# Kernel optimization log

Measured on AMD Instinct MI355X. Metric: run time of the kernel, lower is better.

The kernel has to match this reference:

```python
import jax, jax.numpy as jnp
import numpy as np

EMBED_DIM = 1024
HEAD_DIM = 64
B, T = 4, 4096


def setup_inputs() -> dict:
    key = jax.random.key(0)
    kx, kq, kk, kv = jax.random.split(key, 4)
    x = jax.random.normal(kx, (B, T, EMBED_DIM), dtype=jnp.float32)
    # nn.Linear weights, stored transposed as (in, out) for x @ W
    s = 1.0 / np.sqrt(EMBED_DIM)
    Wq = jax.random.normal(kq, (EMBED_DIM, HEAD_DIM), dtype=jnp.float32) * s
    Wk = jax.random.normal(kk, (EMBED_DIM, HEAD_DIM), dtype=jnp.float32) * s
    Wv = jax.random.normal(kv, (EMBED_DIM, HEAD_DIM), dtype=jnp.float32) * s
    return {"x": x, "Wq": Wq, "Wk": Wk, "Wv": Wv}


def reference(x, Wq, Wk, Wv):
    Bc, Tc, C = x.shape
    Q = x @ Wq  # [B, T, H]
    K = x @ Wk
    V = x @ Wv
    # NOTE: original scales by embedding_dim C, not head_dim
    scores = jnp.einsum('bqh,bkh->bqk', Q, K) / jnp.sqrt(jnp.float32(C))
    causal = jnp.tril(jnp.ones((Tc, Tc), dtype=bool))
    scores = jnp.where(causal, scores, -jnp.inf)
    attn = jax.nn.softmax(scores, axis=-1)
    return jnp.einsum('bqk,bkh->bqh', attn, V)
```

## Files before the change

kernel.cpp:

```cpp
#include <hip/hip_runtime.h>
#include <hip/hip_bf16.h>
#include <math.h>

typedef __attribute__((ext_vector_type(8))) short bf16x8;
typedef __attribute__((ext_vector_type(4))) float f32x4;

#define MFMA16 __builtin_amdgcn_mfma_f32_16x16x32_bf16

static constexpr int TSEQ = 4096;
static constexpr int EMB = 1024;
static constexpr int HD = 64;

__device__ __forceinline__ unsigned short f2bf(float f) {
    unsigned u = __builtin_bit_cast(unsigned, f);
    u += 0x7fffu + ((u >> 16) & 1u);
    return (unsigned short)(u >> 16);
}
__device__ __forceinline__ int pk2bf(float a, float b) {
    return (int)((unsigned)f2bf(a) | ((unsigned)f2bf(b) << 16));
}

union frag_u { int i[4]; bf16x8 v; };

__global__ void prep_w(const float* __restrict__ Wq, const float* __restrict__ Wk,
                       const float* __restrict__ Wv, unsigned short* __restrict__ Wp) {
    int id = blockIdx.x * 256 + threadIdx.x;
    int wsel = id >> 16;
    int t = id & 65535;
    int k = t >> 6, n0 = t & 63;
    const float* W = (wsel == 0) ? Wq : (wsel == 1) ? Wk : Wv;
    float v = W[t];
    if (wsel == 0) v *= 0.03125f;
    int n = wsel * 64 + n0;
    Wp[(k >> 5) * 6144 + n * 32 + (k & 31)] = f2bf(v);
}

__global__ __launch_bounds__(256, 2) void proj_kernel(const float* __restrict__ X,
        const unsigned short* __restrict__ Wp, unsigned short* __restrict__ Qp,
        unsigned short* __restrict__ Kp, unsigned short* __restrict__ Vp) {
    __shared__ unsigned short xt[2][32][64];
    const int tid = threadIdx.x;
    const int lane = tid & 63, wave = tid >> 6;
    const int col = lane & 15, quad = lane >> 4;
    const int rf = wave & 1, ch = wave >> 1;
    const int row0 = blockIdx.x * 32;

    const int srow = tid >> 3;
    const int spiece = tid & 7;
    const float* gx = X + (size_t)(row0 + srow) * EMB + spiece * 8;
    const int sdst = ((spiece ^ (srow & 7)) * 8);

    const int arow = rf * 16 + col;
    const int apu0 = (0 * 4 + quad) ^ (arow & 7);
    const int apu1 = (1 * 4 + quad) ^ (arow & 7);

    const int fragoff = col * 64 + quad * 16;
    const char* wB = (const char*)Wp + ch * 6 * 1024 + fragoff;

    f32x4 acc[6];
#pragma unroll
    for (int t = 0; t < 6; t++) acc[t] = (f32x4)(0.0f);

    {
        const float4 xa = *(const float4*)(gx);
        const float4 xb = *(const float4*)(gx + 4);
        frag_u u;
        u.i[0] = pk2bf(xa.x, xa.y); u.i[1] = pk2bf(xa.z, xa.w);
        u.i[2] = pk2bf(xb.x, xb.y); u.i[3] = pk2bf(xb.z, xb.w);
        *(bf16x8*)&xt[0][srow][sdst] = u.v;
    }
    __syncthreads();

    int buf = 0;
    for (int kc = 0; kc < 16; kc++) {
        float4 xa, xb;
        if (kc < 15) {
            const float* g = gx + (kc + 1) * 64;
            xa = *(const float4*)(g);
            xb = *(const float4*)(g + 4);
        }
        const bf16x8 a0 = *(const bf16x8*)&xt[buf][arow][apu0 * 8];
        const bf16x8 a1 = *(const bf16x8*)&xt[buf][arow][apu1 * 8];
        const char* wp = wB + kc * 24576;
#pragma unroll
        for (int cf = 0; cf < 6; cf++) {
            const bf16x8 w0 = *(const bf16x8*)(wp + cf * 1024);
            const bf16x8 w1 = *(const bf16x8*)(wp + 12288 + cf * 1024);
            acc[cf] = MFMA16(a0, w0, acc[cf], 0, 0, 0);
            acc[cf] = MFMA16(a1, w1, acc[cf], 0, 0, 0);
        }
        if (kc < 15) {
            frag_u u;
            u.i[0] = pk2bf(xa.x, xa.y); u.i[1] = pk2bf(xa.z, xa.w);
            u.i[2] = pk2bf(xb.x, xb.y); u.i[3] = pk2bf(xb.z, xb.w);
            *(bf16x8*)&xt[buf ^ 1][srow][sdst] = u.v;
        }
        __syncthreads();
        buf ^= 1;
    }

    const int tile = blockIdx.x * 2 + rf;
    const int c = blockIdx.x;
    const int j = rf;
#pragma unroll
    for (int cf = 0; cf < 6; cf++) {
        const int n0 = ch * 96 + cf * 16;
        if (n0 < 64) {
            const int t = n0 >> 4;
#pragma unroll
            for (int r = 0; r < 4; r++)
                Qp[tile * 1024 + (t >> 1) * 512 + (quad * 4 + r) * 32 +
                   ((t & 1) * 2 + (col >> 3)) * 8 + (col & 7)] = f2bf(acc[cf][r]);
        } else if (n0 < 128) {
            const int tt = (n0 - 64) >> 4;
#pragma unroll
            for (int r = 0; r < 4; r++)
                Kp[((c * 2 + j) * 2 + (tt >> 1)) * 512 + (quad * 4 + r) * 32 +
                   ((tt & 1) * 2 + (col >> 3)) * 8 + (col & 7)] = f2bf(acc[cf][r]);
        } else {
            const int t4 = (n0 - 128) >> 4;
            ushort4 pk;
            pk.x = f2bf(acc[cf][0]); pk.y = f2bf(acc[cf][1]);
            pk.z = f2bf(acc[cf][2]); pk.w = f2bf(acc[cf][3]);
            *(ushort4*)&Vp[c * 2048 + t4 * 512 + col * 32 + j * 16 + quad * 4] = pk;
        }
    }
}

__global__ __launch_bounds__(512, 4) void attn_kernel(const unsigned short* __restrict__ Qp,
        const unsigned short* __restrict__ Kp, const unsigned short* __restrict__ Vp,
        float* __restrict__ Out) {
    __shared__ float cmb[4][2][64][20];
    __shared__ unsigned short plds[8][2][640];
    const int lane = threadIdx.x & 63, wave = threadIdx.x >> 6;
    const int col = lane & 15, quad = lane >> 4;
    const int batch = blockIdx.x & 3;
    const int ti = 127 - (blockIdx.x >> 2);
    const int q0 = ti * 32;
    const size_t bT = (size_t)batch * TSEQ;
    const int fragoff = col * 64 + quad * 16;

    const char* QpB = (const char*)Qp;
    const char* KpB = (const char*)Kp;
    const char* VpB = (const char*)Vp;
    const int gt = (int)((bT + q0) >> 4);
    const int c0 = (int)(bT >> 5);

    bf16x8 aq[2][2];
#pragma unroll
    for (int m = 0; m < 2; m++)
#pragma unroll
        for (int h = 0; h < 2; h++)
            aq[m][h] = *(const bf16x8*)(QpB + (size_t)((gt + m) * 2 + h) * 1024 + fragoff);

    f32x4 o[2][4];
    f32x4 lsum[2];
#pragma unroll
    for (int m = 0; m < 2; m++) {
        lsum[m] = (f32x4)(0.0f);
#pragma unroll
        for (int t = 0; t < 4; t++) o[m][t] = (f32x4)(0.0f);
    }

    for (int c = wave; c <= ti; c += 8) {
        const char* kb = KpB + (size_t)(c0 + c) * 4096;
        const char* vb = VpB + (size_t)(c0 + c) * 4096;
        bf16x8 bk[2][2], bv[4];
#pragma unroll
        for (int j = 0; j < 2; j++)
#pragma unroll
            for (int h = 0; h < 2; h++)
                bk[j][h] = *(const bf16x8*)(kb + j * 2048 + h * 1024 + fragoff);
#pragma unroll
        for (int t = 0; t < 4; t++)
            bv[t] = *(const bf16x8*)(vb + t * 1024 + fragoff);

        f32x4 s[2][2];
#pragma unroll
        for (int m = 0; m < 2; m++)
#pragma unroll
            for (int j = 0; j < 2; j++) {
                f32x4 a = MFMA16(aq[m][0], bk[j][0], (f32x4)(0.0f), 0, 0, 0);
                s[m][j] = MFMA16(aq[m][1], bk[j][1], a, 0, 0, 0);
            }
        const bool diag = (c == ti);
#pragma unroll
        for (int m = 0; m < 2; m++)
#pragma unroll
            for (int j = 0; j < 2; j++)
#pragma unroll
                for (int r = 0; r < 4; r++) {
                    float v = s[m][j][r];
                    if (diag && (j * 16 + col > m * 16 + quad * 4 + r)) v = -INFINITY;
                    const float p = __expf(v);
                    lsum[m][r] += p;
                    plds[wave][m][(quad * 4 + r) * 40 + j * 16 + col] =
                        (unsigned short)(__builtin_bit_cast(unsigned, p) >> 16);
                }
        bf16x8 pa[2];
#pragma unroll
        for (int m = 0; m < 2; m++)
            pa[m] = *(const bf16x8*)(&plds[wave][m][col * 40 + quad * 8]);
#pragma unroll
        for (int m = 0; m < 2; m++)
#pragma unroll
            for (int t = 0; t < 4; t++)
                o[m][t] = MFMA16(pa[m], bv[t], o[m][t], 0, 0, 0);
    }

    auto wr = [&](int s) {
#pragma unroll
        for (int m = 0; m < 2; m++) {
#pragma unroll
            for (int t = 0; t < 4; t++)
                *(f32x4*)&cmb[s][m][lane][t * 4] = o[m][t];
            *(f32x4*)&cmb[s][m][lane][16] = lsum[m];
        }
    };
    auto rd = [&](int s) {
#pragma unroll
        for (int m = 0; m < 2; m++) {
#pragma unroll
            for (int t = 0; t < 4; t++)
                o[m][t] += *(const f32x4*)&cmb[s][m][lane][t * 4];
            lsum[m] += *(const f32x4*)&cmb[s][m][lane][16];
        }
    };
    if (wave >= 4) wr(wave - 4);
    __syncthreads();
    if (wave < 4) rd(wave);
    __syncthreads();
    if (wave == 2 || wave == 3) wr(wave);
    __syncthreads();
    if (wave < 2) rd(wave + 2);
    __syncthreads();
    if (wave == 1) wr(1);
    __syncthreads();
    if (wave == 0) {
        rd(1);
#pragma unroll
        for (int off = 1; off < 16; off <<= 1)
#pragma unroll
            for (int m = 0; m < 2; m++)
#pragma unroll
                for (int r = 0; r < 4; r++)
                    lsum[m][r] += __shfl_xor(lsum[m][r], off, 64);
#pragma unroll
        for (int m = 0; m < 2; m++)
#pragma unroll
            for (int r = 0; r < 4; r++) {
                const float inv = 1.0f / lsum[m][r];
                const size_t orow = (bT + q0 + m * 16 + quad * 4 + r) * HD;
#pragma unroll
                for (int t = 0; t < 4; t++)
                    Out[orow + t * 16 + col] = o[m][t][r] * inv;
            }
    }
}

extern "C" void kernel_launch(void* const* d_in, const int* in_sizes, int n_in,
                              void* d_out, int out_size, void* d_ws, size_t ws_size,
                              hipStream_t stream) {
    const float* x  = (const float*)d_in[0];
    const float* Wq = (const float*)d_in[1];
    const float* Wk = (const float*)d_in[2];
    const float* Wv = (const float*)d_in[3];
    float* out = (float*)d_out;

    char* w = (char*)d_ws;
    unsigned short* Wp = (unsigned short*)(w);
    unsigned short* Qp = (unsigned short*)(w + (512 << 10));
    unsigned short* Kp = (unsigned short*)(w + (512 << 10) + (2 << 20));
    unsigned short* Vp = (unsigned short*)(w + (512 << 10) + (4 << 20));

    hipLaunchKernelGGL(prep_w, dim3(768), dim3(256), 0, stream, Wq, Wk, Wv, Wp);
    hipLaunchKernelGGL(proj_kernel, dim3(512), dim3(256), 0, stream, x, Wp, Qp, Kp, Vp);
    hipLaunchKernelGGL(attn_kernel, dim3(512), dim3(512), 0, stream, Qp, Kp, Vp, out);
}
```

Measured before the change: 162.6 us.

## Stage projection weights in LDS and retile waves across both row fragments

The projection kernel used to read weight fragments straight from global memory on every k-chunk. Each wave now loads the 192x64 bf16 weight chunk cooperatively into swizzled shared memory alongside the X tile, with a two-deep register prefetch. Waves are retiled so each one computes a 2x3 grid of 16x16 fragments (32 rows by 48 columns) instead of 1x6, which lets each weight and activation fragment read from LDS feed more MFMAs. The trade-off is a larger LDS footprint (about 57KB per block), which may limit occupancy, and more LDS traffic per chunk.

Measured after the change: 200.8 us. 23.5% more time.

```diff
diff --git a/kernel.cpp b/kernel.cpp
--- a/kernel.cpp
+++ b/kernel.cpp
@@ -32,97 +32,115 @@
     float v = W[t];
     if (wsel == 0) v *= 0.03125f;
     int n = wsel * 64 + n0;
-    Wp[(k >> 5) * 6144 + n * 32 + (k & 31)] = f2bf(v);
+    Wp[(k >> 6) * 12288 + n * 64 + (k & 63)] = f2bf(v);
 }
 
 __global__ __launch_bounds__(256, 2) void proj_kernel(const float* __restrict__ X,
         const unsigned short* __restrict__ Wp, unsigned short* __restrict__ Qp,
         unsigned short* __restrict__ Kp, unsigned short* __restrict__ Vp) {
-    __shared__ unsigned short xt[2][32][64];
+    __shared__ unsigned short sb[2][224 * 64];
     const int tid = threadIdx.x;
     const int lane = tid & 63, wave = tid >> 6;
     const int col = lane & 15, quad = lane >> 4;
-    const int rf = wave & 1, ch = wave >> 1;
     const int row0 = blockIdx.x * 32;
 
-    const int srow = tid >> 3;
-    const int spiece = tid & 7;
-    const float* gx = X + (size_t)(row0 + srow) * EMB + spiece * 8;
-    const int sdst = ((spiece ^ (srow & 7)) * 8);
-
-    const int arow = rf * 16 + col;
-    const int apu0 = (0 * 4 + quad) ^ (arow & 7);
-    const int apu1 = (1 * 4 + quad) ^ (arow & 7);
-
-    const int fragoff = col * 64 + quad * 16;
-    const char* wB = (const char*)Wp + ch * 6 * 1024 + fragoff;
-
-    f32x4 acc[6];
-#pragma unroll
-    for (int t = 0; t < 6; t++) acc[t] = (f32x4)(0.0f);
-
-    {
-        const float4 xa = *(const float4*)(gx);
-        const float4 xb = *(const float4*)(gx + 4);
+    const int xrow = tid >> 3, xpc = tid & 7;
+    const float* xg = X + (size_t)(row0 + xrow) * EMB + xpc * 8;
+    const int xw_off = (192 + xrow) * 64 + ((xpc ^ (xrow & 7)) * 8);
+
+    uint4 wreg[2][6];
+    float4 xa[2], xb[2];
+
+    auto load_chunk = [&](int kc, int s) {
+        const unsigned short* wg = Wp + kc * 12288;
+#pragma unroll
+        for (int i = 0; i < 6; i++)
+            wreg[s][i] = *(const uint4*)(wg + (i * 256 + tid) * 8);
+        const float* xp = xg + kc * 64;
+        xa[s] = *(const float4*)(xp);
+        xb[s] = *(const float4*)(xp + 4);
+    };
+    auto write_chunk = [&](int s, int buf) {
+        unsigned short* b = &sb[buf][0];
+#pragma unroll
+        for (int i = 0; i < 6; i++) {
+            const int idx = i * 256 + tid;
+            const int n = idx >> 3, p = idx & 7;
+            *(uint4*)&b[n * 64 + ((p ^ (n & 7)) * 8)] = wreg[s][i];
+        }
         frag_u u;
-        u.i[0] = pk2bf(xa.x, xa.y); u.i[1] = pk2bf(xa.z, xa.w);
-        u.i[2] = pk2bf(xb.x, xb.y); u.i[3] = pk2bf(xb.z, xb.w);
-        *(bf16x8*)&xt[0][srow][sdst] = u.v;
-    }
-    __syncthreads();
-
-    int buf = 0;
+        u.i[0] = pk2bf(xa[s].x, xa[s].y); u.i[1] = pk2bf(xa[s].z, xa[s].w);
+        u.i[2] = pk2bf(xb[s].x, xb[s].y); u.i[3] = pk2bf(xb[s].z, xb[s].w);
+        *(bf16x8*)&b[xw_off] = u.v;
+    };
+
+    f32x4 acc[2][3];
+#pragma unroll
+    for (int af = 0; af < 2; af++)
+#pragma unroll
+        for (int cf = 0; cf < 3; cf++) acc[af][cf] = (f32x4)(0.0f);
+
+    load_chunk(0, 0);
+    write_chunk(0, 0);
+    load_chunk(1, 1);
+    asm volatile("s_waitcnt lgkmcnt(0)\ns_barrier" ::: "memory");
+
     for (int kc = 0; kc < 16; kc++) {
-        float4 xa, xb;
-        if (kc < 15) {
-            const float* g = gx + (kc + 1) * 64;
-            xa = *(const float4*)(g);
-            xb = *(const float4*)(g + 4);
-        }
-        const bf16x8 a0 = *(const bf16x8*)&xt[buf][arow][apu0 * 8];
-        const bf16x8 a1 = *(const bf16x8*)&xt[buf][arow][apu1 * 8];
-        const char* wp = wB + kc * 24576;
-#pragma unroll
-        for (int cf = 0; cf < 6; cf++) {
-            const bf16x8 w0 = *(const bf16x8*)(wp + cf * 1024);
-            const bf16x8 w1 = *(const bf16x8*)(wp + 12288 + cf * 1024);
-            acc[cf] = MFMA16(a0, w0, acc[cf], 0, 0, 0);
-            acc[cf] = MFMA16(a1, w1, acc[cf], 0, 0, 0);
-        }
-        if (kc < 15) {
-            frag_u u;
-            u.i[0] = pk2bf(xa.x, xa.y); u.i[1] = pk2bf(xa.z, xa.w);
-            u.i[2] = pk2bf(xb.x, xb.y); u.i[3] = pk2bf(xb.z, xb.w);
-            *(bf16x8*)&xt[buf ^ 1][srow][sdst] = u.v;
-        }
-        __syncthreads();
-        buf ^= 1;
-    }
-
-    const int tile = blockIdx.x * 2 + rf;
+        const int buf = kc & 1;
+        if (kc < 15) write_chunk((kc + 1) & 1, buf ^ 1);
+        if (kc < 14) load_chunk(kc + 2, kc & 1);
+        const unsigned short* b = &sb[buf][0];
+#pragma unroll
+        for (int j = 0; j < 2; j++) {
+            const int v = j * 4 + quad;
+            bf16x8 a[2], w[3];
+#pragma unroll
+            for (int af = 0; af < 2; af++) {
+                const int r = af * 16 + col;
+                a[af] = *(const bf16x8*)&b[(192 + r) * 64 + ((v ^ (r & 7)) * 8)];
+            }
+#pragma unroll
+            for (int cf = 0; cf < 3; cf++) {
+                const int n = wave * 48 + cf * 16 + col;
+                w[cf] = *(const bf16x8*)&b[n * 64 + ((v ^ (n & 7)) * 8)];
+            }
+#pragma unroll
+            for (int af = 0; af < 2; af++)
+#pragma unroll
+                for (int cf = 0; cf < 3; cf++)
+                    acc[af][cf] = MFMA16(a[af], w[cf], acc[af][cf], 0, 0, 0);
+        }
+        if (kc < 15)
+            asm volatile("s_waitcnt lgkmcnt(0)\ns_barrier" ::: "memory");
+    }
+
     const int c = blockIdx.x;
-    const int j = rf;
-#pragma unroll
-    for (int cf = 0; cf < 6; cf++) {
-        const int n0 = ch * 96 + cf * 16;
-        if (n0 < 64) {
-            const int t = n0 >> 4;
-#pragma unroll
-            for (int r = 0; r < 4; r++)
-                Qp[tile * 1024 + (t >> 1) * 512 + (quad * 4 + r) * 32 +
-                   ((t & 1) * 2 + (col >> 3)) * 8 + (col & 7)] = f2bf(acc[cf][r]);
-        } else if (n0 < 128) {
-            const int tt = (n0 - 64) >> 4;
-#pragma unroll
-            for (int r = 0; r < 4; r++)
-                Kp[((c * 2 + j) * 2 + (tt >> 1)) * 512 + (quad * 4 + r) * 32 +
-                   ((tt & 1) * 2 + (col >> 3)) * 8 + (col & 7)] = f2bf(acc[cf][r]);
-        } else {
-            const int t4 = (n0 - 128) >> 4;
-            ushort4 pk;
-            pk.x = f2bf(acc[cf][0]); pk.y = f2bf(acc[cf][1]);
-            pk.z = f2bf(acc[cf][2]); pk.w = f2bf(acc[cf][3]);
-            *(ushort4*)&Vp[c * 2048 + t4 * 512 + col * 32 + j * 16 + quad * 4] = pk;
+#pragma unroll
+    for (int af = 0; af < 2; af++) {
+        const int tile = c * 2 + af;
+        const int j = af;
+#pragma unroll
+        for (int cf = 0; cf < 3; cf++) {
+            const int n0 = wave * 48 + cf * 16;
+            if (n0 < 64) {
+                const int t = n0 >> 4;
+#pragma unroll
+                for (int r = 0; r < 4; r++)
+                    Qp[tile * 1024 + (t >> 1) * 512 + (quad * 4 + r) * 32 +
+                       ((t & 1) * 2 + (col >> 3)) * 8 + (col & 7)] = f2bf(acc[af][cf][r]);
+            } else if (n0 < 128) {
+                const int tt = (n0 - 64) >> 4;
+#pragma unroll
+                for (int r = 0; r < 4; r++)
+                    Kp[((c * 2 + j) * 2 + (tt >> 1)) * 512 + (quad * 4 + r) * 32 +
+                       ((tt & 1) * 2 + (col >> 3)) * 8 + (col & 7)] = f2bf(acc[af][cf][r]);
+            } else {
+                const int t4 = (n0 - 128) >> 4;
+                ushort4 pk;
+                pk.x = f2bf(acc[af][cf][0]); pk.y = f2bf(acc[af][cf][1]);
+                pk.z = f2bf(acc[af][cf][2]); pk.w = f2bf(acc[af][cf][3]);
+                *(ushort4*)&Vp[c * 2048 + t4 * 512 + col * 32 + j * 16 + quad * 4] = pk;
+            }
         }
     }
 }
```
